# Kernel tuning notes

Measured on AMD Instinct MI355X. Metric: run time of the kernel, lower is better.

The kernel has to match this reference:

```python
import jax, jax.numpy as jnp
import numpy as np

DIMS = [512, 256, 128]   # transformer_dims == graph_embed_dims
DINS = [3, 512, 256]     # per-stage input feature dim (xyz, then prev stage output)
N_SINK = 20

def _lin(k, fi, fo):
    return jax.random.normal(k, (fi, fo), jnp.float32) / np.float32(np.sqrt(fi))

def sinkhorn_rpm(log_alpha, n_iters=N_SINK):
    # slack=True: zero-pad one extra row/col, alternate row/col logsumexp normalization
    la = jnp.pad(log_alpha, ((0, 0), (0, 1), (0, 1)))
    for _ in range(n_iters):
        top = la[:, :-1, :]
        la = jnp.concatenate([top - jax.nn.logsumexp(top, axis=2, keepdims=True), la[:, -1:, :]], axis=1)
        left = la[:, :, :-1]
        la = jnp.concatenate([left - jax.nn.logsumexp(left, axis=1, keepdims=True), la[:, :, -1:]], axis=2)
    return la[:, :-1, :-1]

def _forward(P_src, P_tgt, A_src, A_tgt,
             Wp0, bp0, We0, be0, Wa0, ba0, Wu0, bu0, Aff0, Wc0, bc0,
             Wp1, bp1, We1, be1, Wt1, Wa1, ba1, Wu1, bu1, Aff1, Wc1, bc1,
             Wp2, bp2, We2, be2, Wt2, Wa2, ba2, Wu2, bu2, Aff2, Wc2, bc2):
    Wp = [Wp0, Wp1, Wp2]; bp = [bp0, bp1, bp2]
    We = [We0, We1, We2]; be = [be0, be1, be2]
    Wt = [None, Wt1, Wt2]
    Wa = [Wa0, Wa1, Wa2]; ba = [ba0, ba1, ba2]
    Wu = [Wu0, Wu1, Wu2]; bu = [bu0, bu1, bu2]
    Aff = [Aff0, Aff1, Aff2]
    Wc = [Wc0, Wc1, Wc2]; bc = [bc0, bc1, bc2]
    emb_s, emb_t = P_src, P_tgt
    A_s, A_t = A_src, A_tgt
    s = None
    for i in range(3):
        d = DIMS[i]
        # DGCNN_SDIM stand-in: per-point MLPs for point + edge features, concat to 2d channels
        emb_s = jnp.concatenate([jax.nn.relu(emb_s @ Wp[i] + bp[i]),
                                 jax.nn.relu(emb_s @ We[i] + be[i])], axis=-1)  # [B,N,2d]
        emb_t = jnp.concatenate([jax.nn.relu(emb_t @ Wp[i] + bp[i]),
                                 jax.nn.relu(emb_t @ We[i] + be[i])], axis=-1)
        if i > 0:
            # transformer edge generator -> attention adjacency, per forward():
            # scores = emb^T emb / sqrt(d_k); A = softmax(scores, -1)
            se = emb_s @ Wt[i]  # [B,N,d]
            te = emb_t @ Wt[i]
            inv = np.float32(1.0 / np.sqrt(d))
            A_s = jax.nn.softmax(jnp.einsum('bnd,bmd->bnm', se, se) * inv, axis=-1)
            A_t = jax.nn.softmax(jnp.einsum('bnd,bmd->bnm', te, te) * inv, axis=-1)
        # Siamese Gconv message passing: relu(A (x Wa + ba) + x Wu + bu)
        emb_s = jax.nn.relu(jnp.einsum('bnm,bmd->bnd', A_s, emb_s @ Wa[i] + ba[i]) + emb_s @ Wu[i] + bu[i])
        emb_t = jax.nn.relu(jnp.einsum('bnm,bmd->bnd', A_t, emb_t @ Wa[i] + ba[i]) + emb_t @ Wu[i] + bu[i])
        # affinity (symmetrized bilinear form) + 20-iter slack Sinkhorn
        M = 0.5 * (Aff[i] + Aff[i].T)
        s = jnp.einsum('bnd,de,bme->bnm', emb_s, M, emb_t)
        s = jnp.exp(sinkhorn_rpm(s))
        # cross conv: fuse own features with matched cross features
        emb1 = jnp.concatenate([emb_s, jnp.einsum('bnm,bmd->bnd', s, emb_t)], axis=-1) @ Wc[i] + bc[i]
        emb2 = jnp.concatenate([emb_t, jnp.einsum('bmn,bmd->bnd', s, emb_s)], axis=-1) @ Wc[i] + bc[i]
        emb_s, emb_t = emb1, emb2
        if i < 2:
            # top-k node selection: softmax over nodes, sum channels, keep top DIMS[i] nodes
            k = DIMS[i]
            score_s = jax.nn.softmax(emb_s, axis=1).sum(-1)  # [B,N]
            idx_s = jax.lax.top_k(score_s, k)[1]             # [B,k]
            emb_s = jnp.take_along_axis(emb_s, idx_s[:, :, None], axis=1)
            score_t = jax.nn.softmax(emb_t, axis=1).sum(-1)
            idx_t = jax.lax.top_k(score_t, k)[1]
            emb_t = jnp.take_along_axis(emb_t, idx_t[:, :, None], axis=1)
    return s  # final doubly-stochastic matching matrix [B,256,256]

def setup_inputs():
    B, N = 4, 1024
    key = jax.random.key(0)
    ks = jax.random.split(key, 40)
    inp = {
        'P_src': jax.random.normal(ks[0], (B, N, 3), jnp.float32),
        'P_tgt': jax.random.normal(ks[1], (B, N, 3), jnp.float32),
        'A_src': jax.random.uniform(ks[2], (B, N, N), jnp.float32) / N,
        'A_tgt': jax.random.uniform(ks[3], (B, N, N), jnp.float32) / N,
    }
    ki = 4
    for i in range(3):
        d, di = DIMS[i], DINS[i]
        inp[f'Wp{i}'] = _lin(ks[ki], di, d); ki += 1
        inp[f'bp{i}'] = jnp.zeros((d,), jnp.float32)
        inp[f'We{i}'] = _lin(ks[ki], di, d); ki += 1
        inp[f'be{i}'] = jnp.zeros((d,), jnp.float32)
        if i > 0:
            inp[f'Wt{i}'] = _lin(ks[ki], 2 * d, d); ki += 1
        inp[f'Wa{i}'] = _lin(ks[ki], 2 * d, d); ki += 1
        inp[f'ba{i}'] = jnp.zeros((d,), jnp.float32)
        inp[f'Wu{i}'] = _lin(ks[ki], 2 * d, d); ki += 1
        inp[f'bu{i}'] = jnp.zeros((d,), jnp.float32)
        inp[f'Aff{i}'] = _lin(ks[ki], d, d); ki += 1
        inp[f'Wc{i}'] = _lin(ks[ki], 2 * d, d); ki += 1
        inp[f'bc{i}'] = jnp.zeros((d,), jnp.float32)
    return inp

def reference(P_src, P_tgt, A_src, A_tgt,
              Wp0, bp0, We0, be0, Wa0, ba0, Wu0, bu0, Aff0, Wc0, bc0,
              Wp1, bp1, We1, be1, Wt1, Wa1, ba1, Wu1, bu1, Aff1, Wc1, bc1,
              Wp2, bp2, We2, be2, Wt2, Wa2, ba2, Wu2, bu2, Aff2, Wc2, bc2):
    return _forward(P_src, P_tgt, A_src, A_tgt,
                    Wp0, bp0, We0, be0, Wa0, ba0, Wu0, bu0, Aff0, Wc0, bc0,
                    Wp1, bp1, We1, be1, Wt1, Wa1, ba1, Wu1, bu1, Aff1, Wc1, bc1,
                    Wp2, bp2, We2, be2, Wt2, Wa2, ba2, Wu2, bu2, Aff2, Wc2, bc2)
```

## Files before the change

kernel.cpp:

```cpp
#include <hip/hip_runtime.h>
#include <hip/hip_bf16.h>
#include <math.h>

__device__ inline float bf2f(unsigned short u) { return __uint_as_float(((unsigned)u) << 16); }

__global__ void detect_dtype_k(const unsigned short* __restrict__ src, int* __restrict__ flag) {
  int lane = threadIdx.x & 63;
  unsigned short w = src[2 * lane];
  unsigned e = (w >> 7) & 0xFFu;
  bool inr = (e >= 96u && e <= 130u);
  unsigned long long m = __ballot(inr);
  if (lane == 0) *flag = (__popcll(m) >= 48) ? 1 : 0;
}

struct GemmP {
  const int* dflag;
  const void* A; long long aoff; long long sA; int lda; int tA; int adin;
  const void* B; long long boff; long long sB; int ldb; int tB; int bdin;
  const float* A2; int lda2;
  const void* B2; long long b2off; int ldb2; int K2; int b2din;
  const void* bias;
  const float* add; int ldadd;
  float* C; long long sC; int ldc;
  int M, Nc, K;
  double scale; int relu;
};

__device__ inline unsigned ldbits(const void* p, long long idx, int dyn, int isdin) {
  if (isdin && dyn) return ((unsigned)((const unsigned short*)p)[idx]) << 16;
  return ((const unsigned*)p)[idx];
}

template <int TS, int KS>
__device__ __forceinline__ void gemm_core(const GemmP& p) {
  constexpr int PAD = TS + 4;
  constexpr int RPT = TS / 16;
  constexpr int TPR = 256 / TS;
  constexpr int EPT = TS * KS / 256;
  __shared__ __align__(16) float As[KS][PAD];
  __shared__ __align__(16) float Bs[KS][PAD];
  int dyn = p.dflag[0];
  int bz = blockIdx.z;
  int gx = gridDim.x;
  int nwg = gx * gridDim.y;
  int lin = blockIdx.y * gx + blockIdx.x;
  int q = nwg >> 3, r = nwg & 7;
  int xcd = lin & 7, cidx = lin >> 3;
  int nl = (xcd < r ? xcd * (q + 1) : r * (q + 1) + (xcd - r) * q) + cidx;
  int by = nl / gx;
  int row0 = by * TS, col0 = (nl - by * gx) * TS;
  int t = threadIdx.x;
  int rg = t >> 4, cg = t & 15;

  double acc[RPT][RPT];
#pragma unroll
  for (int i = 0; i < RPT; i++)
#pragma unroll
    for (int j = 0; j < RPT; j++) acc[i][j] = 0.0;
  unsigned apf[EPT], bpf[EPT];

  for (int seg = 0; seg < 2; seg++) {
    const void* Ap; const void* Bp;
    long long aofs, bofs;
    int lda, ldb, tA, tB, K, adin, bdin;
    if (seg == 0) {
      Ap = p.A; aofs = p.aoff + (long long)bz * p.sA; lda = p.lda; tA = p.tA; adin = p.adin;
      Bp = p.B; bofs = p.boff + (long long)bz * p.sB; ldb = p.ldb; tB = p.tB; bdin = p.bdin;
      K = p.K;
    } else {
      if (!p.A2) break;
      Ap = p.A2; aofs = 0; lda = p.lda2; tA = 0; adin = 0;
      Bp = p.B2; bofs = p.b2off; ldb = p.ldb2; tB = 0; bdin = p.b2din;
      K = p.K2;
    }
    int a_loc = tA ? (t % TS) : (t / TPR);
    int a_k0  = tA ? (t / TS) : (t % TPR);
    int am = row0 + a_loc;
    bool a_ok = am < p.M;
    int b_loc = tB ? (t / TPR) : (t % TS);
    int b_k0  = tB ? (t % TPR) : (t / TS);
    int bn = col0 + b_loc;
    bool b_ok = bn < p.Nc;
    int b_pos = (b_loc & 15) * RPT + (b_loc >> 4);
    long long abase = aofs + (tA ? (long long)a_k0 * lda + am : (long long)am * lda + a_k0);
    long long austr = tA ? (long long)TPR * lda : TPR;
    long long astep = tA ? (long long)KS * lda : KS;
    long long bbase = bofs + (tB ? (long long)bn * ldb + b_k0 : (long long)b_k0 * ldb + bn);
    long long bustr = tB ? TPR : (long long)TPR * ldb;
    long long bstep = tB ? KS : (long long)KS * ldb;

    auto LOAD = [&](int k0) {
#pragma unroll
      for (int u = 0; u < EPT; u++) {
        int k = k0 + a_k0 + u * TPR;
        apf[u] = (a_ok && k < K) ? ldbits(Ap, abase + u * austr, dyn, adin) : 0u;
      }
#pragma unroll
      for (int u = 0; u < EPT; u++) {
        int k = k0 + b_k0 + u * TPR;
        bpf[u] = (b_ok && k < K) ? ldbits(Bp, bbase + u * bustr, dyn, bdin) : 0u;
      }
      abase += astep; bbase += bstep;
    };
    auto STORE = [&]() {
#pragma unroll
      for (int u = 0; u < EPT; u++) As[a_k0 + u * TPR][a_loc] = __uint_as_float(apf[u]);
#pragma unroll
      for (int u = 0; u < EPT; u++) Bs[b_k0 + u * TPR][b_pos] = __uint_as_float(bpf[u]);
    };
    int nst = (K + KS - 1) / KS;
    LOAD(0);
    for (int ts = 0; ts < nst; ts++) {
      __syncthreads();
      STORE();
      __syncthreads();
      if (ts + 1 < nst) LOAD((ts + 1) * KS);
#pragma unroll
      for (int kk = 0; kk < KS; kk++) {
        double av[RPT], bv[RPT];
#pragma unroll
        for (int i = 0; i < RPT; i++) av[i] = (double)As[kk][RPT * rg + i];
#pragma unroll
        for (int j = 0; j < RPT; j++) bv[j] = (double)Bs[kk][RPT * cg + j];
#pragma unroll
        for (int i = 0; i < RPT; i++)
#pragma unroll
          for (int j = 0; j < RPT; j++) acc[i][j] = fma(av[i], bv[j], acc[i][j]);
      }
    }
  }
  const float* addb = p.add;
  float* Cb = p.C + (long long)bz * p.sC;
#pragma unroll
  for (int i = 0; i < RPT; i++) {
    int m = row0 + RPT * rg + i;
    if (m >= p.M) continue;
#pragma unroll
    for (int j = 0; j < RPT; j++) {
      int n = col0 + cg + 16 * j;
      if (n >= p.Nc) continue;
      double v = acc[i][j] * p.scale;
      if (p.bias)
        v += dyn ? (double)bf2f(((const unsigned short*)p.bias)[n])
                 : (double)((const float*)p.bias)[n];
      if (addb) v += (double)addb[(long long)m * p.ldadd + n];
      if (p.relu) v = fmax(v, 0.0);
      Cb[(long long)m * p.ldc + n] = (float)v;
    }
  }
}

__launch_bounds__(256, 4)
__global__ void gemm_fx32(GemmP p) { gemm_core<32, 16>(p); }

__launch_bounds__(256, 2)
__global__ void gemm_fx64(GemmP p) { gemm_core<64, 32>(p); }

__launch_bounds__(256)
__global__ void row_softmax_k(float* __restrict__ A, int N) {
  long long row = (long long)blockIdx.x * 4 + (threadIdx.x >> 6);
  int lane = threadIdx.x & 63;
  float* a = A + row * N;
  double ev[8];
  int nc = N >> 6;
  double mx = -INFINITY;
  for (int k = 0; k < nc; k++) mx = fmax(mx, (double)a[lane + (k << 6)]);
  for (int off = 32; off; off >>= 1) mx = fmax(mx, __shfl_xor(mx, off, 64));
  double s = 0.0;
  for (int k = 0; k < nc; k++) { double e = exp((double)a[lane + (k << 6)] - mx); ev[k] = e; s += e; }
  for (int off = 32; off; off >>= 1) s += __shfl_xor(s, off, 64);
  double inv = 1.0 / s;
  for (int k = 0; k < nc; k++) a[lane + (k << 6)] = (float)(ev[k] * inv);
}

__launch_bounds__(256)
__global__ void msym_k(const void* __restrict__ Aff, float* __restrict__ Ms, int d,
                       const int* __restrict__ dflag) {
  int fl = dflag[0];
  int idx = blockIdx.x * 256 + threadIdx.x;
  if (idx < d * d) {
    int i = idx / d, j = idx - i * d;
    double a, b;
    if (fl) {
      a = (double)bf2f(((const unsigned short*)Aff)[idx]);
      b = (double)bf2f(((const unsigned short*)Aff)[j * d + i]);
    } else {
      a = (double)((const float*)Aff)[idx];
      b = (double)((const float*)Aff)[j * d + i];
    }
    Ms[idx] = (float)(0.5 * (a + b));
  }
}

__launch_bounds__(256)
__global__ void sink_u_k(const float* __restrict__ S, const double* __restrict__ V,
                         double* __restrict__ U, int N) {
  extern __shared__ double vsh[];
  int b = blockIdx.y;
  const float* Sb = S + (long long)b * N * N;
  const double* Vb = V + (long long)b * N;
  int tid = threadIdx.x, lane = tid & 63, wv = tid >> 6;
  for (int c = tid; c < N; c += 256) vsh[c] = Vb[c];
  __syncthreads();
  int row = blockIdx.x * 4 + wv;
  const float* Sr = Sb + (long long)row * N;
  double m = (lane == 0) ? 0.0 : -INFINITY;
  double s = (lane == 0) ? 1.0 : 0.0;
  for (int c = lane; c < N; c += 64) {
    double x = (double)Sr[c] - vsh[c];
    if (x > m) { s = s * exp(m - x) + 1.0; m = x; }
    else s += exp(x - m);
  }
  for (int off = 32; off; off >>= 1) {
    double mo = __shfl_xor(m, off, 64);
    double so = __shfl_xor(s, off, 64);
    double mm = fmax(m, mo);
    s = s * exp(m - mm) + so * exp(mo - mm);
    m = mm;
  }
  if (lane == 0) U[(long long)b * N + row] = m + log(s);
}

__launch_bounds__(256)
__global__ void sink_v_k(const float* __restrict__ S, const double* __restrict__ U,
                         double* __restrict__ V, int N) {
  extern __shared__ double ush[];
  double* mred = ush + N;
  double* sred = mred + 256;
  int b = blockIdx.y;
  const float* Sb = S + (long long)b * N * N;
  int tid = threadIdx.x, cl = tid & 15, rg = tid >> 4;
  int c = blockIdx.x * 16 + cl;
  for (int i = tid; i < N; i += 256) ush[i] = U[(long long)b * N + i];
  __syncthreads();
  double m = (rg == 0) ? 0.0 : -INFINITY;
  double s = (rg == 0) ? 1.0 : 0.0;
  for (int i = rg; i < N; i += 16) {
    double x = (double)Sb[(long long)i * N + c] - ush[i];
    if (x > m) { s = s * exp(m - x) + 1.0; m = x; }
    else s += exp(x - m);
  }
  mred[rg * 16 + cl] = m; sred[rg * 16 + cl] = s;
  __syncthreads();
  if (rg == 0) {
    for (int g = 1; g < 16; g++) {
      double mo = mred[g * 16 + cl], so = sred[g * 16 + cl];
      double mm = fmax(m, mo);
      s = s * exp(m - mm) + so * exp(mo - mm);
      m = mm;
    }
    V[(long long)b * N + c] = m + log(s);
  }
}

__launch_bounds__(256)
__global__ void sink_p_k(const float* __restrict__ S, const double* __restrict__ U,
                         const double* __restrict__ V, float* __restrict__ P, int N) {
  int b = blockIdx.y;
  long long base = (long long)b * N * N;
  const double* Ub = U + (long long)b * N;
  const double* Vb = V + (long long)b * N;
  for (long long e = (long long)blockIdx.x * 256 + threadIdx.x; e < (long long)N * N;
       e += (long long)gridDim.x * 256) {
    int i = (int)(e / N), j = (int)(e - (long long)i * N);
    P[base + e] = (float)exp((double)S[base + e] - Ub[i] - Vb[j]);
  }
}

__launch_bounds__(256)
__global__ void colstats_k(const float* __restrict__ emb, double* __restrict__ stats, int N, int d) {
  int g = blockIdx.y;
  int cl = threadIdx.x & 63;
  int c = blockIdx.x * 64 + cl;
  int rg = threadIdx.x >> 6;
  const float* e = emb + (long long)g * N * d;
  __shared__ double redm[4][64];
  __shared__ double reds[4][64];
  double mx = -INFINITY;
  for (int r = rg; r < N; r += 4) mx = fmax(mx, (double)e[(long long)r * d + c]);
  redm[rg][cl] = mx;
  __syncthreads();
  mx = fmax(fmax(redm[0][cl], redm[1][cl]), fmax(redm[2][cl], redm[3][cl]));
  __syncthreads();
  double s = 0.0;
  for (int r = rg; r < N; r += 4) s += exp((double)e[(long long)r * d + c] - mx);
  reds[rg][cl] = s;
  __syncthreads();
  if (rg == 0) {
    s = reds[0][cl] + reds[1][cl] + reds[2][cl] + reds[3][cl];
    stats[((long long)g * d + c) * 2] = mx;
    stats[((long long)g * d + c) * 2 + 1] = 1.0 / s;
  }
}

__launch_bounds__(256)
__global__ void score_k(const float* __restrict__ emb, const double* __restrict__ stats,
                        double* __restrict__ score, int N, int d) {
  int g = blockIdx.y;
  int r = blockIdx.x * 64 + (threadIdx.x >> 2);
  int sub = threadIdx.x & 3;
  const float* e = emb + ((long long)g * N + r) * d;
  const double* st = stats + (long long)g * d * 2;
  double s = 0.0;
  for (int c = sub; c < d; c += 4) s += exp((double)e[c] - st[2 * c]) * st[2 * c + 1];
  s += __shfl_down(s, 2, 4);
  s += __shfl_down(s, 1, 4);
  if (sub == 0) score[(long long)g * N + r] = (double)(float)s;
}

__launch_bounds__(256)
__global__ void topk_sort_k(const double* __restrict__ score, int* __restrict__ SIDX,
                            int N, int k) {
  __shared__ double sv[1024];
  __shared__ int si[1024];
  int g = blockIdx.x, tid = threadIdx.x;
  (void)k;
  for (int i = tid; i < N; i += 256) { sv[i] = score[(long long)g * N + i]; si[i] = i; }
  __syncthreads();
  for (int kk = 2; kk <= N; kk <<= 1) {
    for (int j = kk >> 1; j > 0; j >>= 1) {
      for (int i = tid; i < N; i += 256) {
        int ixj = i ^ j;
        if (ixj > i) {
          double v1 = sv[i], v2 = sv[ixj];
          int x1 = si[i], x2 = si[ixj];
          bool gtr = (v1 < v2) || (v1 == v2 && x1 > x2);
          bool up = ((i & kk) == 0);
          if (gtr == up) { sv[i] = v2; sv[ixj] = v1; si[i] = x2; si[ixj] = x1; }
        }
      }
      __syncthreads();
    }
  }
  for (int i = tid; i < N; i += 256) SIDX[(long long)g * N + i] = si[i];
}

__launch_bounds__(256)
__global__ void gather_k(const int* __restrict__ SIDX, const float* __restrict__ emb,
                         float* __restrict__ out, int N, int d, int k) {
  int g = blockIdx.y;
  int total = k * d;
  const int* sx = SIDX + (long long)g * N;
  const float* eb = emb + (long long)g * N * d;
  float* ob = out + (long long)g * total;
  int stride = gridDim.x * 256;
  int e0 = blockIdx.x * 256 + threadIdx.x;
  int r = e0 / d, c = e0 - r * d;
  int rs = stride / d, cs = stride - rs * d;
  for (int e = e0; e < total; e += stride) {
    ob[e] = eb[(long long)sx[r] * d + c];
    r += rs; c += cs;
    if (c >= d) { c -= d; r += 1; }
  }
}

__launch_bounds__(256)
__global__ void cvt_out_k(const float* __restrict__ src, void* __restrict__ dst,
                          long long oofs, int n, const int* __restrict__ dflag) {
  int fl = dflag[0];
  int i = blockIdx.x * 256 + threadIdx.x;
  if (i < n) {
    float v = src[i];
    if (fl) ((__hip_bfloat16*)dst)[oofs + i] = __float2bfloat16(v);
    else ((float*)dst)[oofs + i] = v;
  }
}

extern "C" void kernel_launch(void* const* d_in, const int* in_sizes, int n_in,
                              void* d_out, int out_size, void* d_ws, size_t ws_size,
                              hipStream_t stream) {
  (void)in_sizes; (void)n_in; (void)out_size;
  static const int NL[3] = {1024, 512, 256};
  static const int DL[3] = {512, 256, 128};
  static const int DINL[3] = {3, 512, 256};
  static const int IWp[3]={0,11,23}, IBp[3]={1,12,24}, IWe[3]={2,13,25}, IBe[3]={3,14,26};
  static const int IWt[3]={-1,15,27};
  static const int IWa[3]={4,16,28}, IBa[3]={5,17,29}, IWu[3]={6,18,30}, IBu[3]={7,19,31};
  static const int IAff[3]={8,20,32}, IWc[3]={9,21,33}, IBc[3]={10,22,34};

  auto Wv = [&](int t) { return (const void*)d_in[4 + t]; };

  float* ws = (float*)d_ws;
  const long long PER_PC = 5257232LL;
  int pc = 1;
  if (ws_size >= (size_t)(PER_PC * 4 * 4 + 64)) pc = 4;
  else if (ws_size >= (size_t)(PER_PC * 2 * 4 + 64)) pc = 2;

  float* A0 = ws;
  float* B0 = A0 + 2097152LL * pc;
  float* C0 = B0 + 1048576LL * pc;
  float* D0 = C0 + 1048576LL * pc;
  float* IN = D0 + 524288LL * pc;
  double* ST = (double*)(IN + 524288LL * pc);
  double* SC = ST + 2048LL * pc;
  double* SU = SC + 2048LL * pc;
  double* SV = SU + 1024LL * pc;
  int* SIDX = (int*)(SV + 1024LL * pc);
  int* FLAG = SIDX + 2048LL * pc;

  detect_dtype_k<<<dim3(1), dim3(64), 0, stream>>>((const unsigned short*)d_in[0], FLAG);

  GemmP p_;
  auto gemm = [&](const void* A, long long aoff, long long sA, int lda, int tA, int adin,
                  const void* B, long long boff, long long sB, int ldb, int tB, int bdin,
                  const float* A2, int lda2,
                  const void* B2, long long b2off, int ldb2, int K2, int b2din,
                  const void* bias, const float* add, int ldadd,
                  float* C, long long sC, int ldc, int M, int Nc, int K,
                  double scale, int relu, int batches) {
    p_.dflag = FLAG;
    p_.A = A; p_.aoff = aoff; p_.sA = sA; p_.lda = lda; p_.tA = tA; p_.adin = adin;
    p_.B = B; p_.boff = boff; p_.sB = sB; p_.ldb = ldb; p_.tB = tB; p_.bdin = bdin;
    p_.A2 = A2; p_.lda2 = lda2;
    p_.B2 = B2; p_.b2off = b2off; p_.ldb2 = ldb2; p_.K2 = K2; p_.b2din = b2din;
    p_.bias = bias; p_.add = add; p_.ldadd = ldadd;
    p_.C = C; p_.sC = sC; p_.ldc = ldc; p_.M = M; p_.Nc = Nc; p_.K = K;
    p_.scale = scale; p_.relu = relu;
    long long b64 = (long long)((Nc + 63) / 64) * ((M + 63) / 64) * batches;
    if (b64 >= 384) {
      dim3 grid((Nc + 63) / 64, (M + 63) / 64, batches);
      gemm_fx64<<<grid, dim3(256), 0, stream>>>(p_);
    } else {
      dim3 grid((Nc + 31) / 32, (M + 31) / 32, batches);
      gemm_fx32<<<grid, dim3(256), 0, stream>>>(p_);
    }
  };

  for (int p0 = 0; p0 < 4; p0 += pc) {
    const int s = 2 * pc;
    for (int L = 0; L < 3; L++) {
      int N = NL[L], d = DL[L], din = DINL[L];
      long long ns = (long long)N * d, NN = (long long)N * N;
      int sN = s * N, pcN = pc * N;
      float* X2 = A0;
      float* H = B0;
      float* X3 = C0;
      float* Af = D0;
      float* Spt = A0;
      float* Ppt = A0 + (long long)pc * NN;
      float* G = B0;
      float* MSp = B0 + (long long)pc * ns;
      float* Y = B0;
      float* EMB = A0;

      if (L == 0) {
        long long poff = (long long)p0 * N * 3;
        float* X2t = X2 + (long long)pcN * 2 * d;
        gemm(d_in[0],poff,0,3,0,1, Wv(IWp[0]),0,0,d,0,1, nullptr,0, nullptr,0,0,0,0,
             Wv(IBp[0]), nullptr,0, X2, 0, 2*d, pcN, d, 3, 1.0, 1, 1);
        gemm(d_in[0],poff,0,3,0,1, Wv(IWe[0]),0,0,d,0,1, nullptr,0, nullptr,0,0,0,0,
             Wv(IBe[0]), nullptr,0, X2 + d, 0, 2*d, pcN, d, 3, 1.0, 1, 1);
        gemm(d_in[1],poff,0,3,0,1, Wv(IWp[0]),0,0,d,0,1, nullptr,0, nullptr,0,0,0,0,
             Wv(IBp[0]), nullptr,0, X2t, 0, 2*d, pcN, d, 3, 1.0, 1, 1);
        gemm(d_in[1],poff,0,3,0,1, Wv(IWe[0]),0,0,d,0,1, nullptr,0, nullptr,0,0,0,0,
             Wv(IBe[0]), nullptr,0, X2t + d, 0, 2*d, pcN, d, 3, 1.0, 1, 1);
      } else {
        gemm(IN,0,0,din,0,0, Wv(IWp[L]),0,0,d,0,1, nullptr,0, nullptr,0,0,0,0,
             Wv(IBp[L]), nullptr,0, X2, 0, 2*d, sN, d, din, 1.0, 1, 1);
        gemm(IN,0,0,din,0,0, Wv(IWe[L]),0,0,d,0,1, nullptr,0, nullptr,0,0,0,0,
             Wv(IBe[L]), nullptr,0, X2 + d, 0, 2*d, sN, d, din, 1.0, 1, 1);
      }
      if (L > 0) {
        float* SE = B0;
        double inv = (double)(float)(1.0 / sqrt((double)d));
        gemm(X2,0,0,2*d,0,0, Wv(IWt[L]),0,0,d,0,1, nullptr,0, nullptr,0,0,0,0,
             nullptr, nullptr,0, SE, 0, d, sN, d, 2*d, 1.0, 0, 1);
        gemm(SE,0,ns,d,0,0, SE,0,ns,d,1,0, nullptr,0, nullptr,0,0,0,0,
             nullptr, nullptr,0, Af, NN, N, N, N, d, inv, 0, s);
        row_softmax_k<<<dim3(sN / 4), dim3(256), 0, stream>>>(Af, N);
      }
      gemm(X2,0,0,2*d,0,0, Wv(IWa[L]),0,0,d,0,1, nullptr,0, nullptr,0,0,0,0,
           Wv(IBa[L]), nullptr,0, H, 0, d, sN, d, 2*d, 1.0, 0, 1);
      if (L == 0) {
        gemm(d_in[2],(long long)p0*NN,NN,N,0,1, H,0,ns,d,0,0, nullptr,0, nullptr,0,0,0,0,
             nullptr, nullptr,0, X3, ns, d, N, d, N, 1.0, 0, pc);
        gemm(d_in[3],(long long)p0*NN,NN,N,0,1, H + (long long)pc*ns,0,ns,d,0,0, nullptr,0, nullptr,0,0,0,0,
             nullptr, nullptr,0, X3 + (long long)pc*ns, ns, d, N, d, N, 1.0, 0, pc);
      } else {
        gemm(Af,0,NN,N,0,0, H,0,ns,d,0,0, nullptr,0, nullptr,0,0,0,0,
             nullptr, nullptr,0, X3, ns, d, N, d, N, 1.0, 0, s);
      }
      gemm(X2,0,0,2*d,0,0, Wv(IWu[L]),0,0,d,0,1, nullptr,0, nullptr,0,0,0,0,
           Wv(IBu[L]), X3,d, X3, 0, d, sN, d, 2*d, 1.0, 1, 1);
      msym_k<<<dim3((d * d + 255) / 256), dim3(256), 0, stream>>>(Wv(IAff[L]), MSp, d, FLAG);
      gemm(X3 + (long long)pc*ns,0,0,d,0,0, MSp,0,0,d,0,0, nullptr,0, nullptr,0,0,0,0,
           nullptr, nullptr,0, G, 0, d, pcN, d, d, 1.0, 0, 1);
      gemm(X3,0,ns,d,0,0, G,0,ns,d,1,0, nullptr,0, nullptr,0,0,0,0,
           nullptr, nullptr,0, Spt, NN, N, N, N, d, 1.0, 0, pc);
      hipMemsetAsync(SV, 0, (size_t)pc * N * sizeof(double), stream);
      for (int it = 0; it < 20; it++) {
        sink_u_k<<<dim3(N / 4, pc), dim3(256), N * sizeof(double), stream>>>(Spt, SV, SU, N);
        sink_v_k<<<dim3(N / 16, pc), dim3(256), (N + 512) * sizeof(double), stream>>>(Spt, SU, SV, N);
      }
      sink_p_k<<<dim3(256, pc), dim3(256), 0, stream>>>(Spt, SU, SV, Ppt, N);
      if (L == 2) {
        int on = pc * 65536;
        cvt_out_k<<<dim3((on + 255) / 256), dim3(256), 0, stream>>>(
            Ppt, d_out, (long long)p0 * 65536, on, FLAG);
      } else {
        gemm(Ppt,0,NN,N,0,0, X3 + (long long)pc*ns,0,ns,d,0,0, nullptr,0, nullptr,0,0,0,0,
             nullptr, nullptr,0, Y, ns, d, N, d, N, 1.0, 0, pc);
        gemm(Ppt,0,NN,N,1,0, X3,0,ns,d,0,0, nullptr,0, nullptr,0,0,0,0,
             nullptr, nullptr,0, Y + (long long)pc*ns, ns, d, N, d, N, 1.0, 0, pc);
        gemm(X3,0,0,d,0,0, Wv(IWc[L]),0,0,d,0,1, Y,d, Wv(IWc[L]),(long long)d*d,d,d,1,
             Wv(IBc[L]), nullptr,0, EMB, 0, d, sN, d, d, 1.0, 0, 1);
        colstats_k<<<dim3(d / 64, s), dim3(256), 0, stream>>>(EMB, ST, N, d);
        score_k<<<dim3(N / 64, s), dim3(256), 0, stream>>>(EMB, ST, SC, N, d);
        topk_sort_k<<<dim3(s), dim3(256), 0, stream>>>(SC, SIDX, N, N / 2);
        gather_k<<<dim3(128, s), dim3(256), 0, stream>>>(SIDX, EMB, IN, N, d, N / 2);
      }
    }
  }
}
```

Measured before the change: 4.428 ms.

## Use FP64 MFMA matrix cores in the 64-tile GEMM with a runtime layout probe

Replaces the scalar double-precision FMA inner loop of the 64x64 GEMM with __builtin_amdgcn_mfma_f64_16x16x4f64 calls. A one-wave probe kernel works out the MFMA operand and output lane mapping at runtime, checks it on a small test product, and falls back to the scalar path if the check fails. The kernel also remaps workgroups so that consecutive tiles are grouped per XCD. It costs one extra tiny launch per call and adds table lookups in the epilogue.

```diff
diff --git a/kernel.cpp b/kernel.cpp
--- a/kernel.cpp
+++ b/kernel.cpp
@@ -3,6 +3,62 @@
 #include <math.h>
 
 __device__ inline float bf2f(unsigned short u) { return __uint_as_float(((unsigned)u) << 16); }
+
+typedef double f64x4 __attribute__((ext_vector_type(4)));
+
+__device__ int g_tab[520];
+
+__global__ void mfma_probe_k() {
+  int l = threadIdx.x;
+  if (l >= 64) return;
+  double p4[16];
+  p4[0] = 1.0;
+  for (int i = 1; i < 16; i++) p4[i] = p4[i - 1] * 4.0;
+  f64x4 z; z[0] = 0.0; z[1] = 0.0; z[2] = 0.0; z[3] = 0.0;
+  int ok = 1;
+  int ln = l & 15, kg = l >> 4;
+  f64x4 d1 = __builtin_amdgcn_mfma_f64_16x16x4f64(p4[ln], 1.0, z, 0, 0, 0);
+  f64x4 d2 = __builtin_amdgcn_mfma_f64_16x16x4f64(1.0, p4[ln], z, 0, 0, 0);
+  int sig[4];
+  for (int t = 0; t < 4; t++) {
+    f64x4 dt = __builtin_amdgcn_mfma_f64_16x16x4f64((kg == t) ? 1.0 : 0.0, p4[kg], z, 0, 0, 0);
+    int e = -1;
+    for (int i = 0; i < 4; i++)
+      if (dt[0] == p4[i]) e = i;
+    if (e < 0) ok = 0;
+    sig[t] = (e < 0) ? t : e;
+  }
+  int invs[4] = {0, 1, 2, 3};
+  for (int t = 0; t < 4; t++) invs[sig[t]] = t;
+  int rt[4], ct[4];
+  for (int v = 0; v < 4; v++) {
+    int ri = -1, ci = -1;
+    for (int i = 0; i < 16; i++) {
+      if (d1[v] == 4.0 * p4[i]) ri = i;
+      if (d2[v] == 4.0 * p4[i]) ci = i;
+    }
+    if (ri < 0 || ci < 0) ok = 0;
+    rt[v] = (ri < 0) ? 0 : ri;
+    ct[v] = (ci < 0) ? 0 : ci;
+  }
+  double av = (double)(((ln * 3 + kg * 5) % 7) - 3);
+  double bv = (double)(((invs[kg] * 11 + ln * 2) % 5) - 2);
+  f64x4 dd = __builtin_amdgcn_mfma_f64_16x16x4f64(av, bv, z, 0, 0, 0);
+  for (int v = 0; v < 4; v++) {
+    int i = rt[v], j = ct[v];
+    double ex = 0.0;
+    for (int k = 0; k < 4; k++)
+      ex += (double)(((i * 3 + k * 5) % 7) - 3) * (double)(((k * 11 + j * 2) % 5) - 2);
+    if (dd[v] != ex) ok = 0;
+  }
+  unsigned long long allok = __ballot(ok != 0);
+  for (int v = 0; v < 4; v++) {
+    g_tab[l * 4 + v] = rt[v];
+    g_tab[256 + l * 4 + v] = ct[v];
+  }
+  if (l < 4) g_tab[512 + l] = invs[l];
+  if (l == 0) g_tab[516] = (allok == ~0ULL) ? 1 : 0;
+}
 
 __global__ void detect_dtype_k(const unsigned short* __restrict__ src, int* __restrict__ flag) {
   int lane = threadIdx.x & 63;
@@ -154,7 +210,169 @@
 __global__ void gemm_fx32(GemmP p) { gemm_core<32, 16>(p); }
 
 __launch_bounds__(256, 2)
-__global__ void gemm_fx64(GemmP p) { gemm_core<64, 32>(p); }
+__global__ void gemm_fx64(GemmP p) {
+  constexpr int TS = 64, KS = 32, PAD = 68, TPR = 4, EPT = 8;
+  __shared__ __align__(16) float As[KS][PAD];
+  __shared__ __align__(16) float Bs[KS][PAD];
+  int dyn = p.dflag[0];
+  int ok = g_tab[516];
+  int bz = blockIdx.z;
+  int gx = gridDim.x;
+  int nwg = gx * gridDim.y;
+  int lin = blockIdx.y * gx + blockIdx.x;
+  int q = nwg >> 3, r = nwg & 7;
+  int xcd = lin & 7, cidx = lin >> 3;
+  int nl = (xcd < r ? xcd * (q + 1) : r * (q + 1) + (xcd - r) * q) + cidx;
+  int by = nl / gx;
+  int row0 = by * TS, col0 = (nl - by * gx) * TS;
+  int t = threadIdx.x;
+  int lane = t & 63, wv = t >> 6;
+  int ln = lane & 15, kg = lane >> 4;
+  int wm = (wv >> 1) << 5, wn = (wv & 1) << 5;
+  int myinv = g_tab[512 + kg];
+  int rg = t >> 4, cg = t & 15;
+
+  f64x4 acc0, acc1, acc2, acc3;
+#pragma unroll
+  for (int v = 0; v < 4; v++) { acc0[v] = 0.0; acc1[v] = 0.0; acc2[v] = 0.0; acc3[v] = 0.0; }
+  unsigned apf[EPT], bpf[EPT];
+
+  for (int seg = 0; seg < 2; seg++) {
+    const void* Ap; const void* Bp;
+    long long aofs, bofs;
+    int lda, ldb, tA, tB, K, adin, bdin;
+    if (seg == 0) {
+      Ap = p.A; aofs = p.aoff + (long long)bz * p.sA; lda = p.lda; tA = p.tA; adin = p.adin;
+      Bp = p.B; bofs = p.boff + (long long)bz * p.sB; ldb = p.ldb; tB = p.tB; bdin = p.bdin;
+      K = p.K;
+    } else {
+      if (!p.A2) break;
+      Ap = p.A2; aofs = 0; lda = p.lda2; tA = 0; adin = 0;
+      Bp = p.B2; bofs = p.b2off; ldb = p.ldb2; tB = 0; bdin = p.b2din;
+      K = p.K2;
+    }
+    int a_loc = tA ? (t % TS) : (t / TPR);
+    int a_k0  = tA ? (t / TS) : (t % TPR);
+    int am = row0 + a_loc;
+    bool a_okb = am < p.M;
+    int b_loc = tB ? (t / TPR) : (t % TS);
+    int b_k0  = tB ? (t % TPR) : (t / TS);
+    int bn = col0 + b_loc;
+    bool b_okb = bn < p.Nc;
+    long long abase = aofs + (tA ? (long long)a_k0 * lda + am : (long long)am * lda + a_k0);
+    long long austr = tA ? (long long)TPR * lda : TPR;
+    long long astep = tA ? (long long)KS * lda : KS;
+    long long bbase = bofs + (tB ? (long long)bn * ldb + b_k0 : (long long)b_k0 * ldb + bn);
+    long long bustr = tB ? TPR : (long long)TPR * ldb;
+    long long bstep = tB ? KS : (long long)KS * ldb;
+
+    auto LOAD = [&](int k0) {
+#pragma unroll
+      for (int u = 0; u < EPT; u++) {
+        int k = k0 + a_k0 + u * TPR;
+        apf[u] = (a_okb && k < K) ? ldbits(Ap, abase + u * austr, dyn, adin) : 0u;
+      }
+#pragma unroll
+      for (int u = 0; u < EPT; u++) {
+        int k = k0 + b_k0 + u * TPR;
+        bpf[u] = (b_okb && k < K) ? ldbits(Bp, bbase + u * bustr, dyn, bdin) : 0u;
+      }
+      abase += astep; bbase += bstep;
+    };
+    auto STORE = [&]() {
+#pragma unroll
+      for (int u = 0; u < EPT; u++) As[a_k0 + u * TPR][a_loc] = __uint_as_float(apf[u]);
+#pragma unroll
+      for (int u = 0; u < EPT; u++) Bs[b_k0 + u * TPR][b_loc] = __uint_as_float(bpf[u]);
+    };
+    int nst = (K + KS - 1) / KS;
+    LOAD(0);
+    for (int ts = 0; ts < nst; ts++) {
+      __syncthreads();
+      STORE();
+      __syncthreads();
+      if (ts + 1 < nst) LOAD((ts + 1) * KS);
+      if (ok) {
+#pragma unroll
+        for (int g4 = 0; g4 < KS / 4; g4++) {
+          int kb = g4 << 2;
+          double a0 = (double)As[kb + kg][wm + ln];
+          double a1 = (double)As[kb + kg][wm + 16 + ln];
+          double b0 = (double)Bs[kb + myinv][wn + ln];
+          double b1 = (double)Bs[kb + myinv][wn + 16 + ln];
+          acc0 = __builtin_amdgcn_mfma_f64_16x16x4f64(a0, b0, acc0, 0, 0, 0);
+          acc1 = __builtin_amdgcn_mfma_f64_16x16x4f64(a0, b1, acc1, 0, 0, 0);
+          acc2 = __builtin_amdgcn_mfma_f64_16x16x4f64(a1, b0, acc2, 0, 0, 0);
+          acc3 = __builtin_amdgcn_mfma_f64_16x16x4f64(a1, b1, acc3, 0, 0, 0);
+        }
+      } else {
+#pragma unroll
+        for (int kk = 0; kk < KS; kk++) {
+          double av[4], bv[4];
+#pragma unroll
+          for (int i = 0; i < 4; i++) av[i] = (double)As[kk][4 * rg + i];
+#pragma unroll
+          for (int j = 0; j < 4; j++) bv[j] = (double)Bs[kk][cg + 16 * j];
+#pragma unroll
+          for (int j = 0; j < 4; j++) {
+            acc0[j] = fma(av[0], bv[j], acc0[j]);
+            acc1[j] = fma(av[1], bv[j], acc1[j]);
+            acc2[j] = fma(av[2], bv[j], acc2[j]);
+            acc3[j] = fma(av[3], bv[j], acc3[j]);
+          }
+        }
+      }
+    }
+  }
+  const float* addb = p.add;
+  float* Cb = p.C + (long long)bz * p.sC;
+  if (ok) {
+    int rtv[4], ctv[4];
+#pragma unroll
+    for (int v = 0; v < 4; v++) {
+      rtv[v] = g_tab[lane * 4 + v];
+      ctv[v] = g_tab[256 + lane * 4 + v];
+    }
+#pragma unroll
+    for (int rr = 0; rr < 2; rr++) {
+#pragma unroll
+      for (int cc = 0; cc < 2; cc++) {
+#pragma unroll
+        for (int v = 0; v < 4; v++) {
+          int m = row0 + wm + rr * 16 + rtv[v];
+          int n = col0 + wn + cc * 16 + ctv[v];
+          if (m >= p.M || n >= p.Nc) continue;
+          double val = (rr == 0 ? (cc == 0 ? acc0[v] : acc1[v])
+                               : (cc == 0 ? acc2[v] : acc3[v])) * p.scale;
+          if (p.bias)
+            val += dyn ? (double)bf2f(((const unsigned short*)p.bias)[n])
+                       : (double)((const float*)p.bias)[n];
+          if (addb) val += (double)addb[(long long)m * p.ldadd + n];
+          if (p.relu) val = fmax(val, 0.0);
+          Cb[(long long)m * p.ldc + n] = (float)val;
+        }
+      }
+    }
+  } else {
+#pragma unroll
+    for (int i = 0; i < 4; i++) {
+      int m = row0 + 4 * rg + i;
+      if (m >= p.M) continue;
+#pragma unroll
+      for (int j = 0; j < 4; j++) {
+        int n = col0 + cg + 16 * j;
+        if (n >= p.Nc) continue;
+        double v = (i == 0 ? acc0[j] : i == 1 ? acc1[j] : i == 2 ? acc2[j] : acc3[j]) * p.scale;
+        if (p.bias)
+          v += dyn ? (double)bf2f(((const unsigned short*)p.bias)[n])
+                   : (double)((const float*)p.bias)[n];
+        if (addb) v += (double)addb[(long long)m * p.ldadd + n];
+        if (p.relu) v = fmax(v, 0.0);
+        Cb[(long long)m * p.ldc + n] = (float)v;
+      }
+    }
+  }
+}
 
 __launch_bounds__(256)
 __global__ void row_softmax_k(float* __restrict__ A, int N) {
@@ -398,6 +616,7 @@
   int* SIDX = (int*)(SV + 1024LL * pc);
   int* FLAG = SIDX + 2048LL * pc;
 
+  mfma_probe_k<<<dim3(1), dim3(64), 0, stream>>>();
   detect_dtype_k<<<dim3(1), dim3(64), 0, stream>>>((const unsigned short*)d_in[0], FLAG);
 
   GemmP p_;
```

After: 4.061 ms. -8.3%, faster.
